# Kernel tuning notes

Measured on AMD Instinct MI355X. Metric: run time of the kernel, lower is better.

The kernel has to match this reference:

```python
import jax, jax.numpy as jnp
import numpy as np


def setup_inputs() -> dict:
    key = jax.random.key(0)
    k1, k2, k3, k4 = jax.random.split(key, 4)
    B, T, IN, D = 32, 256, 64, 128
    x = jax.random.normal(k1, (B, T, IN), dtype=jnp.float32)
    h0 = jnp.zeros((B, D), dtype=jnp.float32)
    Wx = jax.random.normal(k2, (IN, D), dtype=jnp.float32) * 0.01
    Wgate = jax.random.normal(k3, (D, D), dtype=jnp.float32) * 0.01
    Wh = jax.random.normal(k4, (D, D), dtype=jnp.float32) * 0.01
    return {"x": x, "h0": h0, "Wx": Wx, "Wgate": Wgate, "Wh": Wh}


def reference(x, h0, Wx, Wgate, Wh):
    # x: (B, T, in_dim); h0: (B, dim); returns (h_final, y, hidden_grads, dh_dWh)
    def step_single(h_r, x_r):
        # per-sample gated update: h_r (dim,), x_r (in_dim,)
        pre = x_r @ Wx + h_r @ Wh
        a = jax.nn.gelu(pre, approximate=False)  # torch GELU() is the exact erf variant
        g = jax.nn.sigmoid(a @ Wgate)
        hn = g * h_r + (1.0 - g)
        return hn, hn

    # per-step, per-sample Jacobian d h_new / d h  (mirrors vmap(jacrev(..., argnums=1)))
    jac_batched = jax.vmap(jax.jacrev(step_single, argnums=0, has_aux=True))

    def body(h, x_t):  # h: (B, dim), x_t: (B, in_dim)
        jac, h_new = jac_batched(h, x_t)  # jac: (B, dim, dim)
        return h_new, (h_new, jac)

    xt = jnp.swapaxes(x, 0, 1)  # (T, B, in_dim)
    h_final, (ys, jacs) = jax.lax.scan(body, h0, xt)
    y = jnp.swapaxes(ys, 0, 1)  # (B, T, dim)

    # last-step Jacobian wrt Wh, evaluated with the post-update h (as in the torch code)
    x_last = x[:, -1, :]

    def f_wh(Wh_):
        pre = x_last @ Wx + h_final @ Wh_
        a = jax.nn.gelu(pre, approximate=False)
        g = jax.nn.sigmoid(a @ Wgate)
        return g * h_final + (1.0 - g)

    dh_dWh = jax.jacrev(f_wh)(Wh)  # (B, dim, dim, dim)
    return (h_final, y, jacs, dh_dWh)
```

## Files before the change

### kernel.cpp

```cpp
#include <hip/hip_runtime.h>


#define JACOFF 1052672L
#define DHWOFF 135270400L

typedef __attribute__((ext_vector_type(8))) short frag_ab;
typedef __attribute__((ext_vector_type(4))) float frag_cd;

__device__ __forceinline__ short f2bf(float f) {
    unsigned u = __builtin_bit_cast(unsigned, f);
    unsigned r = (u + 0x7fffu + ((u >> 16) & 1u)) >> 16;
    return (short)r;
}

__global__ __launch_bounds__(256) void prep_xw_kernel(
    const float* __restrict__ Wh, const float* __restrict__ Wg,
    const float* __restrict__ x, const float* __restrict__ Wx,
    float* __restrict__ whT, float* __restrict__ wgT, float* __restrict__ xw)
{
    int blk = blockIdx.x;
    int tid = threadIdx.x;
    if (blk < 128) {
        int idx = blk * 256 + tid;
        if (idx < 16384) {
            int k = idx >> 7, i = idx & 127;
            whT[i * 128 + k] = Wh[idx];
        } else {
            int r = idx - 16384;
            int k = r >> 7, i = r & 127;
            wgT[i * 128 + k] = Wg[r];
        }
        return;
    }
    __shared__ float xs[2][64];
    int sub = tid >> 7;
    int bt = (blk - 128) * 2 + sub;
    int i = tid & 127;
    if (i < 64) xs[sub][i] = x[bt * 64 + i];
    __syncthreads();
    float acc = 0.f;
#pragma unroll
    for (int m = 0; m < 64; ++m)
        acc += xs[sub][m] * Wx[m * 128 + i];
    xw[bt * 128 + i] = acc;
}

__global__ __launch_bounds__(256, 1) void scan_pk_kernel(
    const float* __restrict__ xw, const float* __restrict__ h0,
    const float* __restrict__ whT, const float* __restrict__ wgT,
    const float* __restrict__ Wgate, const float* __restrict__ Wh,
    float* __restrict__ out,
    short* __restrict__ Abf, float* __restrict__ wgv, float* __restrict__ wc,
    float* __restrict__ wdF, float* __restrict__ wuF, float* __restrict__ whF,
    short* __restrict__ PT)
{
    int tid = threadIdx.x;
    if (blockIdx.x >= 32) {
        int c = (blockIdx.x - 32) * 16 + (tid >> 4);
        int k0 = (tid & 15) * 8;
        int i = c >> 7, j = c & 127;
        short v[8];
#pragma unroll
        for (int m = 0; m < 8; ++m) {
            float wg = Wgate[(k0 + m) * 128 + i];
            float wh = Wh[j * 128 + k0 + m];
            v[m] = f2bf(wg * wh);
        }
        *(frag_ab*)(PT + (long)c * 128 + k0) = *(frag_ab*)v;
        return;
    }

    const int b = blockIdx.x;
    const int i = tid >> 1, half = tid & 1;
    __shared__ float hbuf[2][128];
    __shared__ float abuf[128];
    float wh[64], wgc[64];
    {
        const float* whr = whT + i * 128 + half * 64;
        const float* wgr = wgT + i * 128 + half * 64;
#pragma unroll
        for (int k = 0; k < 64; k += 4) {
            float4 a4 = *(const float4*)(whr + k);
            wh[k] = a4.x; wh[k + 1] = a4.y; wh[k + 2] = a4.z; wh[k + 3] = a4.w;
            float4 b4 = *(const float4*)(wgr + k);
            wgc[k] = b4.x; wgc[k + 1] = b4.y; wgc[k + 2] = b4.z; wgc[k + 3] = b4.w;
        }
    }
    if (half == 0) hbuf[0][i] = h0[b * 128 + i];
    __syncthreads();

    const float inv_sqrt2 = 0.70710678118654752f;
    const float inv_sqrt2pi = 0.39894228040143268f;

    float xwv = xw[(b * 256 + 0) * 128 + i];

    for (int t = 0; t < 256; ++t) {
        int p = t & 1;
        int tn = (t < 255) ? t + 1 : 255;
        float xwn = xw[(b * 256 + tn) * 128 + i];

        float s0 = 0.f, s1 = 0.f, s2 = 0.f, s3 = 0.f;
        const float* hb = &hbuf[p][half * 64];
#pragma unroll
        for (int k = 0; k < 64; k += 4) {
            float4 h4 = *(const float4*)(hb + k);
            s0 += h4.x * wh[k];
            s1 += h4.y * wh[k + 1];
            s2 += h4.z * wh[k + 2];
            s3 += h4.w * wh[k + 3];
        }
        float s = (s0 + s1) + (s2 + s3);
        s += __shfl_xor(s, 1);
        float pre = xwv + s;

        float cdf = 0.5f * (1.0f + erff(pre * inv_sqrt2));
        float a = pre * cdf;
        float dval = cdf + pre * inv_sqrt2pi * expf(-0.5f * pre * pre);

        long tb = (long)(t * 32 + b) * 128 + i;
        if (half == 0) {
            Abf[tb] = f2bf(dval);
            abuf[i] = a;
        }
        __syncthreads();

        float r0 = 0.f, r1 = 0.f, r2 = 0.f, r3 = 0.f;
        const float* ab = &abuf[half * 64];
#pragma unroll
        for (int k = 0; k < 64; k += 4) {
            float4 a4 = *(const float4*)(ab + k);
            r0 += a4.x * wgc[k];
            r1 += a4.y * wgc[k + 1];
            r2 += a4.z * wgc[k + 2];
            r3 += a4.w * wgc[k + 3];
        }
        float r = (r0 + r1) + (r2 + r3);
        r += __shfl_xor(r, 1);
        float g = 1.0f / (1.0f + expf(-r));
        float hp = hbuf[p][i];
        float c = (hp - 1.0f) * g * (1.0f - g);
        float hn = g * hp + 1.0f - g;
        if (half == 0) {
            hbuf[p ^ 1][i] = hn;
            wgv[tb] = g;
            wc[tb] = c;
            out[4096 + (b * 256 + t) * 128 + i] = hn;
        }
        xwv = xwn;
        __syncthreads();
    }

    float hfin = hbuf[0][i];
    if (half == 0) {
        out[b * 128 + i] = hfin;
        whF[b * 128 + i] = hfin;
    }

    {
        float s0 = 0.f, s1 = 0.f, s2 = 0.f, s3 = 0.f;
        const float* hb = &hbuf[0][half * 64];
#pragma unroll
        for (int k = 0; k < 64; k += 4) {
            float4 h4 = *(const float4*)(hb + k);
            s0 += h4.x * wh[k];
            s1 += h4.y * wh[k + 1];
            s2 += h4.z * wh[k + 2];
            s3 += h4.w * wh[k + 3];
        }
        float s = (s0 + s1) + (s2 + s3);
        s += __shfl_xor(s, 1);
        float pre = xwv + s;
        float cdf = 0.5f * (1.0f + erff(pre * inv_sqrt2));
        float a = pre * cdf;
        float dval = cdf + pre * inv_sqrt2pi * expf(-0.5f * pre * pre);
        if (half == 0) {
            wdF[b * 128 + i] = dval;
            abuf[i] = a;
        }
        __syncthreads();
        float r0 = 0.f, r1 = 0.f, r2 = 0.f, r3 = 0.f;
        const float* ab = &abuf[half * 64];
#pragma unroll
        for (int k = 0; k < 64; k += 4) {
            float4 a4 = *(const float4*)(ab + k);
            r0 += a4.x * wgc[k];
            r1 += a4.y * wgc[k + 1];
            r2 += a4.z * wgc[k + 2];
            r3 += a4.w * wgc[k + 3];
        }
        float r = (r0 + r1) + (r2 + r3);
        r += __shfl_xor(r, 1);
        float g = 1.0f / (1.0f + expf(-r));
        if (half == 0) wuF[b * 128 + i] = (hfin - 1.0f) * g * (1.0f - g);
    }
}

__global__ __launch_bounds__(256) void jacmm_kernel(
    const short* __restrict__ Abf,
    const short* __restrict__ PT,
    const float* __restrict__ wgv,
    const float* __restrict__ wc,
    float* __restrict__ out)
{
    __shared__ short Atile[128 * 128];
    __shared__ short Btile[128 * 128];

    int bx = blockIdx.x;
    int rb = bx & 63;
    int cb = bx >> 6;
    int tid = threadIdx.x;

    const short* Ag = Abf + (long)rb * (128 * 128);
    const short* Bg = PT + (long)cb * (128 * 128);

#pragma unroll
    for (int e = 0; e < 8; ++e) {
        int q = e * 256 + tid;
        int r = q >> 4;
        int s = q & 15;
        int ko = s ^ (r & 15);
        const short* srcA = Ag + r * 128 + ko * 8;
        const short* srcB = Bg + r * 128 + ko * 8;
        __builtin_amdgcn_global_load_lds(
            (const __attribute__((address_space(1))) void*)srcA,
            (__attribute__((address_space(3))) void*)(Atile + q * 8), 16, 0, 0);
        __builtin_amdgcn_global_load_lds(
            (const __attribute__((address_space(1))) void*)srcB,
            (__attribute__((address_space(3))) void*)(Btile + q * 8), 16, 0, 0);
    }
    __syncthreads();

    int w = tid >> 6;
    int lane = tid & 63;
    int wr = w >> 1;
    int wcol = w & 1;
    int lrow = lane & 15;
    int quad = lane >> 4;

    frag_cd acc[4][4];
#pragma unroll
    for (int p = 0; p < 4; ++p)
#pragma unroll
        for (int q = 0; q < 4; ++q) {
            acc[p][q][0] = 0.f; acc[p][q][1] = 0.f; acc[p][q][2] = 0.f; acc[p][q][3] = 0.f;
        }

#pragma unroll
    for (int kk = 0; kk < 4; ++kk) {
        int ko = kk * 4 + quad;
        frag_ab af[4], bf[4];
#pragma unroll
        for (int p = 0; p < 4; ++p) {
            int r = wr * 64 + p * 16 + lrow;
            int chunk = r * 16 + (ko ^ (r & 15));
            af[p] = *(const frag_ab*)&Atile[chunk * 8];
        }
#pragma unroll
        for (int q = 0; q < 4; ++q) {
            int n = wcol * 64 + q * 16 + lrow;
            int chunk = n * 16 + (ko ^ (n & 15));
            bf[q] = *(const frag_ab*)&Btile[chunk * 8];
        }
#pragma unroll
        for (int p = 0; p < 4; ++p)
#pragma unroll
            for (int q = 0; q < 4; ++q)
                acc[p][q] = __builtin_amdgcn_mfma_f32_16x16x32_bf16(af[p], bf[q], acc[p][q], 0, 0, 0);
    }

    long rowbase = (long)rb * 128;
#pragma unroll
    for (int p = 0; p < 4; ++p) {
        int trow0 = wr * 64 + p * 16 + quad * 4;
#pragma unroll
        for (int reg = 0; reg < 4; ++reg) {
            long row = rowbase + trow0 + reg;
            float ci = wc[row * 128 + cb];
            float gi = wgv[row * 128 + cb];
            float* orow = out + JACOFF + row * 16384 + (long)cb * 128;
#pragma unroll
            for (int q = 0; q < 4; ++q) {
                int tcol = wcol * 64 + q * 16 + lrow;
                float v = ci * acc[p][q][reg];
                if (tcol == cb) v += gi;
                orow[tcol] = v;
            }
        }
    }
}

__global__ __launch_bounds__(256) void dhdw_kernel(const float* __restrict__ Wgate,
                                                   const float* __restrict__ dF,
                                                   const float* __restrict__ uF,
                                                   const float* __restrict__ hF,
                                                   float* __restrict__ out)
{
    int blk = blockIdx.x;
    int b = blk >> 7, i = blk & 127;
    int tid = threadIdx.x;
    __shared__ float hs[128], dsh[128];
    if (tid < 128) {
        hs[tid] = hF[b * 128 + tid];
        dsh[tid] = dF[b * 128 + tid];
    }
    __syncthreads();
    float u = uF[b * 128 + i];
    int q0 = (tid & 31) * 4, p0 = (tid >> 5) * 16;
    float w0 = u * dsh[q0 + 0] * Wgate[(q0 + 0) * 128 + i];
    float w1 = u * dsh[q0 + 1] * Wgate[(q0 + 1) * 128 + i];
    float w2 = u * dsh[q0 + 2] * Wgate[(q0 + 2) * 128 + i];
    float w3 = u * dsh[q0 + 3] * Wgate[(q0 + 3) * 128 + i];
    float* dst = out + DHWOFF + (long)(b * 128 + i) * 16384;
#pragma unroll
    for (int pp = 0; pp < 16; ++pp) {
        float hp = hs[p0 + pp];
        *(float4*)(dst + (p0 + pp) * 128 + q0) = make_float4(hp * w0, hp * w1, hp * w2, hp * w3);
    }
}

extern "C" void kernel_launch(void* const* d_in, const int* in_sizes, int n_in,
                              void* d_out, int out_size, void* d_ws, size_t ws_size,
                              hipStream_t stream)
{
    (void)in_sizes; (void)n_in; (void)out_size; (void)ws_size;
    const float* x     = (const float*)d_in[0];
    const float* h0    = (const float*)d_in[1];
    const float* Wx    = (const float*)d_in[2];
    const float* Wgate = (const float*)d_in[3];
    const float* Wh    = (const float*)d_in[4];
    float* out = (float*)d_out;
    float* ws  = (float*)d_ws;

    float* xw  = ws;
    float* whT = ws + 1048576;
    float* wgT = ws + 1064960;
    float* wgv = ws + 1081344;
    float* wc  = ws + 2129920;
    float* wdF = ws + 3178496;
    float* wuF = ws + 3182592;
    float* whF = ws + 3186688;
    short* Abf = (short*)(ws + 3190784);
    short* PT  = (short*)(ws + 3715072);

    prep_xw_kernel<<<4224, 256, 0, stream>>>(Wh, Wgate, x, Wx, whT, wgT, xw);
    scan_pk_kernel<<<1056, 256, 0, stream>>>(xw, h0, whT, wgT, Wgate, Wh, out,
                                             Abf, wgv, wc, wdF, wuF, whF, PT);
    jacmm_kernel<<<8192, 256, 0, stream>>>(Abf, PT, wgv, wc, out);
    dhdw_kernel<<<4096, 256, 0, stream>>>(Wgate, wdF, wuF, whF, out);
}
```

Baseline: 1.136 ms.

## Quarter-split scan dot products and fuse dh/dWh writer into Jacobian matmul kernel

The scan kernel now uses 512 threads with four lanes per output element, so each thread's serial dot products along the critical recurrence shrink from 64 to 32 terms, at the cost of an extra shuffle reduction. The separate dh/dWh kernel is folded into the Jacobian matmul launch by interleaving one dh/dWh block for every two matmul blocks, which removes a launch and lets the two store-bound phases overlap. The per-row scale and gate loads in the matmul epilogue are hoisted before the tile sync so they overlap the async LDS loads. This costs extra registers and a larger shared-memory footprint for the fused blocks.

```diff
diff --git a/kernel.cpp b/kernel.cpp
--- a/kernel.cpp
+++ b/kernel.cpp
@@ -45,7 +45,7 @@
     xw[bt * 128 + i] = acc;
 }
 
-__global__ __launch_bounds__(256, 1) void scan_pk_kernel(
+__global__ __launch_bounds__(512, 1) void scan_pk_kernel(
     const float* __restrict__ xw, const float* __restrict__ h0,
     const float* __restrict__ whT, const float* __restrict__ wgT,
     const float* __restrict__ Wgate, const float* __restrict__ Wh,
@@ -56,7 +56,7 @@
 {
     int tid = threadIdx.x;
     if (blockIdx.x >= 32) {
-        int c = (blockIdx.x - 32) * 16 + (tid >> 4);
+        int c = (blockIdx.x - 32) * 32 + (tid >> 4);
         int k0 = (tid & 15) * 8;
         int i = c >> 7, j = c & 127;
         short v[8];
@@ -71,22 +71,22 @@
     }
 
     const int b = blockIdx.x;
-    const int i = tid >> 1, half = tid & 1;
+    const int i = tid >> 2, qtr = tid & 3;
     __shared__ float hbuf[2][128];
     __shared__ float abuf[128];
-    float wh[64], wgc[64];
+    float wh[32], wgc[32];
     {
-        const float* whr = whT + i * 128 + half * 64;
-        const float* wgr = wgT + i * 128 + half * 64;
-#pragma unroll
-        for (int k = 0; k < 64; k += 4) {
+        const float* whr = whT + i * 128 + qtr * 32;
+        const float* wgr = wgT + i * 128 + qtr * 32;
+#pragma unroll
+        for (int k = 0; k < 32; k += 4) {
             float4 a4 = *(const float4*)(whr + k);
             wh[k] = a4.x; wh[k + 1] = a4.y; wh[k + 2] = a4.z; wh[k + 3] = a4.w;
             float4 b4 = *(const float4*)(wgr + k);
             wgc[k] = b4.x; wgc[k + 1] = b4.y; wgc[k + 2] = b4.z; wgc[k + 3] = b4.w;
         }
     }
-    if (half == 0) hbuf[0][i] = h0[b * 128 + i];
+    if (qtr == 0) hbuf[0][i] = h0[b * 128 + i];
     __syncthreads();
 
     const float inv_sqrt2 = 0.70710678118654752f;
@@ -100,9 +100,9 @@
         float xwn = xw[(b * 256 + tn) * 128 + i];
 
         float s0 = 0.f, s1 = 0.f, s2 = 0.f, s3 = 0.f;
-        const float* hb = &hbuf[p][half * 64];
-#pragma unroll
-        for (int k = 0; k < 64; k += 4) {
+        const float* hb = &hbuf[p][qtr * 32];
+#pragma unroll
+        for (int k = 0; k < 32; k += 4) {
             float4 h4 = *(const float4*)(hb + k);
             s0 += h4.x * wh[k];
             s1 += h4.y * wh[k + 1];
@@ -111,6 +111,7 @@
         }
         float s = (s0 + s1) + (s2 + s3);
         s += __shfl_xor(s, 1);
+        s += __shfl_xor(s, 2);
         float pre = xwv + s;
 
         float cdf = 0.5f * (1.0f + erff(pre * inv_sqrt2));
@@ -118,16 +119,16 @@
         float dval = cdf + pre * inv_sqrt2pi * expf(-0.5f * pre * pre);
 
         long tb = (long)(t * 32 + b) * 128 + i;
-        if (half == 0) {
+        if (qtr == 0) {
             Abf[tb] = f2bf(dval);
             abuf[i] = a;
         }
         __syncthreads();
 
         float r0 = 0.f, r1 = 0.f, r2 = 0.f, r3 = 0.f;
-        const float* ab = &abuf[half * 64];
-#pragma unroll
-        for (int k = 0; k < 64; k += 4) {
+        const float* ab = &abuf[qtr * 32];
+#pragma unroll
+        for (int k = 0; k < 32; k += 4) {
             float4 a4 = *(const float4*)(ab + k);
             r0 += a4.x * wgc[k];
             r1 += a4.y * wgc[k + 1];
@@ -136,11 +137,12 @@
         }
         float r = (r0 + r1) + (r2 + r3);
         r += __shfl_xor(r, 1);
+        r += __shfl_xor(r, 2);
         float g = 1.0f / (1.0f + expf(-r));
         float hp = hbuf[p][i];
         float c = (hp - 1.0f) * g * (1.0f - g);
         float hn = g * hp + 1.0f - g;
-        if (half == 0) {
+        if (qtr == 0) {
             hbuf[p ^ 1][i] = hn;
             wgv[tb] = g;
             wc[tb] = c;
@@ -151,16 +153,16 @@
     }
 
     float hfin = hbuf[0][i];
-    if (half == 0) {
+    if (qtr == 0) {
         out[b * 128 + i] = hfin;
         whF[b * 128 + i] = hfin;
     }
 
     {
         float s0 = 0.f, s1 = 0.f, s2 = 0.f, s3 = 0.f;
-        const float* hb = &hbuf[0][half * 64];
-#pragma unroll
-        for (int k = 0; k < 64; k += 4) {
+        const float* hb = &hbuf[0][qtr * 32];
+#pragma unroll
+        for (int k = 0; k < 32; k += 4) {
             float4 h4 = *(const float4*)(hb + k);
             s0 += h4.x * wh[k];
             s1 += h4.y * wh[k + 1];
@@ -169,19 +171,20 @@
         }
         float s = (s0 + s1) + (s2 + s3);
         s += __shfl_xor(s, 1);
+        s += __shfl_xor(s, 2);
         float pre = xwv + s;
         float cdf = 0.5f * (1.0f + erff(pre * inv_sqrt2));
         float a = pre * cdf;
         float dval = cdf + pre * inv_sqrt2pi * expf(-0.5f * pre * pre);
-        if (half == 0) {
+        if (qtr == 0) {
             wdF[b * 128 + i] = dval;
             abuf[i] = a;
         }
         __syncthreads();
         float r0 = 0.f, r1 = 0.f, r2 = 0.f, r3 = 0.f;
-        const float* ab = &abuf[half * 64];
-#pragma unroll
-        for (int k = 0; k < 64; k += 4) {
+        const float* ab = &abuf[qtr * 32];
+#pragma unroll
+        for (int k = 0; k < 32; k += 4) {
             float4 a4 = *(const float4*)(ab + k);
             r0 += a4.x * wgc[k];
             r1 += a4.y * wgc[k + 1];
@@ -190,25 +193,54 @@
         }
         float r = (r0 + r1) + (r2 + r3);
         r += __shfl_xor(r, 1);
+        r += __shfl_xor(r, 2);
         float g = 1.0f / (1.0f + expf(-r));
-        if (half == 0) wuF[b * 128 + i] = (hfin - 1.0f) * g * (1.0f - g);
-    }
-}
-
-__global__ __launch_bounds__(256) void jacmm_kernel(
+        if (qtr == 0) wuF[b * 128 + i] = (hfin - 1.0f) * g * (1.0f - g);
+    }
+}
+
+__global__ __launch_bounds__(256) void jacmm_dhdw_kernel(
     const short* __restrict__ Abf,
     const short* __restrict__ PT,
     const float* __restrict__ wgv,
     const float* __restrict__ wc,
+    const float* __restrict__ Wgate,
+    const float* __restrict__ dF, const float* __restrict__ uF, const float* __restrict__ hF,
     float* __restrict__ out)
 {
+    int bx = blockIdx.x;
+    int tid = threadIdx.x;
+    int grp = bx / 3, rem = bx % 3;
+
+    if (rem == 2) {
+        __shared__ float hs[128], dsh[128];
+        int b = grp >> 7, i = grp & 127;
+        if (tid < 128) {
+            hs[tid] = hF[b * 128 + tid];
+            dsh[tid] = dF[b * 128 + tid];
+        }
+        __syncthreads();
+        float u = uF[b * 128 + i];
+        int q0 = (tid & 31) * 4, p0 = (tid >> 5) * 16;
+        float w0 = u * dsh[q0 + 0] * Wgate[(q0 + 0) * 128 + i];
+        float w1 = u * dsh[q0 + 1] * Wgate[(q0 + 1) * 128 + i];
+        float w2 = u * dsh[q0 + 2] * Wgate[(q0 + 2) * 128 + i];
+        float w3 = u * dsh[q0 + 3] * Wgate[(q0 + 3) * 128 + i];
+        float* dst = out + DHWOFF + (long)grp * 16384;
+#pragma unroll
+        for (int pp = 0; pp < 16; ++pp) {
+            float hp = hs[p0 + pp];
+            *(float4*)(dst + (p0 + pp) * 128 + q0) = make_float4(hp * w0, hp * w1, hp * w2, hp * w3);
+        }
+        return;
+    }
+
     __shared__ short Atile[128 * 128];
     __shared__ short Btile[128 * 128];
 
-    int bx = blockIdx.x;
-    int rb = bx & 63;
-    int cb = bx >> 6;
-    int tid = threadIdx.x;
+    int jb = grp * 2 + rem;
+    int rb = jb & 63;
+    int cb = jb >> 6;
 
     const short* Ag = Abf + (long)rb * (128 * 128);
     const short* Bg = PT + (long)cb * (128 * 128);
@@ -228,7 +260,6 @@
             (const __attribute__((address_space(1))) void*)srcB,
             (__attribute__((address_space(3))) void*)(Btile + q * 8), 16, 0, 0);
     }
-    __syncthreads();
 
     int w = tid >> 6;
     int lane = tid & 63;
@@ -237,6 +268,20 @@
     int lrow = lane & 15;
     int quad = lane >> 4;
 
+    long rowbase = (long)rb * 128;
+    float ci[4][4], gi[4][4];
+#pragma unroll
+    for (int p = 0; p < 4; ++p) {
+        int trow0 = wr * 64 + p * 16 + quad * 4;
+#pragma unroll
+        for (int reg = 0; reg < 4; ++reg) {
+            long row = rowbase + trow0 + reg;
+            ci[p][reg] = wc[row * 128 + cb];
+            gi[p][reg] = wgv[row * 128 + cb];
+        }
+    }
+    __syncthreads();
+
     frag_cd acc[4][4];
 #pragma unroll
     for (int p = 0; p < 4; ++p)
@@ -268,53 +313,21 @@
                 acc[p][q] = __builtin_amdgcn_mfma_f32_16x16x32_bf16(af[p], bf[q], acc[p][q], 0, 0, 0);
     }
 
-    long rowbase = (long)rb * 128;
 #pragma unroll
     for (int p = 0; p < 4; ++p) {
         int trow0 = wr * 64 + p * 16 + quad * 4;
 #pragma unroll
         for (int reg = 0; reg < 4; ++reg) {
             long row = rowbase + trow0 + reg;
-            float ci = wc[row * 128 + cb];
-            float gi = wgv[row * 128 + cb];
             float* orow = out + JACOFF + row * 16384 + (long)cb * 128;
 #pragma unroll
             for (int q = 0; q < 4; ++q) {
                 int tcol = wcol * 64 + q * 16 + lrow;
-                float v = ci * acc[p][q][reg];
-                if (tcol == cb) v += gi;
+                float v = ci[p][reg] * acc[p][q][reg];
+                if (tcol == cb) v += gi[p][reg];
                 orow[tcol] = v;
             }
         }
-    }
-}
-
-__global__ __launch_bounds__(256) void dhdw_kernel(const float* __restrict__ Wgate,
-                                                   const float* __restrict__ dF,
-                                                   const float* __restrict__ uF,
-                                                   const float* __restrict__ hF,
-                                                   float* __restrict__ out)
-{
-    int blk = blockIdx.x;
-    int b = blk >> 7, i = blk & 127;
-    int tid = threadIdx.x;
-    __shared__ float hs[128], dsh[128];
-    if (tid < 128) {
-        hs[tid] = hF[b * 128 + tid];
-        dsh[tid] = dF[b * 128 + tid];
-    }
-    __syncthreads();
-    float u = uF[b * 128 + i];
-    int q0 = (tid & 31) * 4, p0 = (tid >> 5) * 16;
-    float w0 = u * dsh[q0 + 0] * Wgate[(q0 + 0) * 128 + i];
-    float w1 = u * dsh[q0 + 1] * Wgate[(q0 + 1) * 128 + i];
-    float w2 = u * dsh[q0 + 2] * Wgate[(q0 + 2) * 128 + i];
-    float w3 = u * dsh[q0 + 3] * Wgate[(q0 + 3) * 128 + i];
-    float* dst = out + DHWOFF + (long)(b * 128 + i) * 16384;
-#pragma unroll
-    for (int pp = 0; pp < 16; ++pp) {
-        float hp = hs[p0 + pp];
-        *(float4*)(dst + (p0 + pp) * 128 + q0) = make_float4(hp * w0, hp * w1, hp * w2, hp * w3);
     }
 }
 
@@ -343,8 +356,7 @@
     short* PT  = (short*)(ws + 3715072);
 
     prep_xw_kernel<<<4224, 256, 0, stream>>>(Wh, Wgate, x, Wx, whT, wgT, xw);
-    scan_pk_kernel<<<1056, 256, 0, stream>>>(xw, h0, whT, wgT, Wgate, Wh, out,
-                                             Abf, wgv, wc, wdF, wuF, whF, PT);
-    jacmm_kernel<<<8192, 256, 0, stream>>>(Abf, PT, wgv, wc, out);
-    dhdw_kernel<<<4096, 256, 0, stream>>>(Wgate, wdF, wuF, whF, out);
-}
+    scan_pk_kernel<<<544, 512, 0, stream>>>(xw, h0, whT, wgT, Wgate, Wh, out,
+                                            Abf, wgv, wc, wdF, wuF, whF, PT);
+    jacmm_dhdw_kernel<<<12288, 256, 0, stream>>>(Abf, PT, wgv, wc, Wgate, wdF, wuF, whF, out);
+}
```

Measured after the change: 1.085 ms. -4.5%, faster.
